# Kernel optimization log

Hardware: AMD Instinct MI355X
Metric: run time of the kernel (lower is better)

Reference implementation:

```python
import jax, jax.numpy as jnp
import numpy as np

H = 8  # num_heads

def setup_inputs() -> dict:
    key = jax.random.key(0)
    k1, k2, k3, k4 = jax.random.split(key, 4)
    B, T, D, K = 16, 8192, 512, 4
    x = jax.random.normal(k1, (B, T, D), dtype=jnp.float32)
    mask = jax.random.randint(k2, (B, T), 0, 2, dtype=jnp.int32)
    queries = jax.random.normal(k3, (1, K, D), dtype=jnp.float32) * 0.02
    # xavier_uniform for (D, D) Linear weight
    limit = np.sqrt(6.0 / (D + D))
    w_out = jax.random.uniform(k4, (D, D), dtype=jnp.float32, minval=-limit, maxval=limit)
    b_out = jnp.zeros((D,), dtype=jnp.float32)
    return {"x": x, "mask": mask, "queries": queries, "w_out": w_out, "b_out": b_out}

def reference(x, mask, queries, w_out, b_out):
    B, T, D = x.shape
    K = queries.shape[1]
    hd = D // H
    scale = jnp.sqrt(jnp.float32(hd))
    q = queries.reshape(K, H, hd)          # shared across batch
    kv = x.reshape(B, T, H, hd)            # keys == values
    scores = jnp.einsum('khd,bthd->bhkt', q, kv) / scale  # (B,H,K,T)
    scores = jnp.where(mask[:, None, None, :] == 0, jnp.float32(-1e9), scores)
    attn = jax.nn.softmax(scores, axis=-1)  # dropout is identity in eval / p=0
    out = jnp.einsum('bhkt,bthd->bkhd', attn, kv).reshape(B, K, D)
    return out @ w_out.T + b_out
```

## Files before the change

### kernel.cpp

```cpp
#include <hip/hip_runtime.h>
#include <math.h>

#define BB 16
#define TT 8192
#define DD 512
#define KK 4
#define HH 8
#define HD 64

__global__ __launch_bounds__(256, 2)
void attn_partial_kernel(const float* __restrict__ x,
                         const int* __restrict__ mask,
                         const float* __restrict__ queries,
                         float* __restrict__ ws,
                         int NC) {
    const int C     = TT / NC;
    const int iters = C >> 3;
    const int b     = blockIdx.x / NC;
    const int c     = blockIdx.x % NC;
    const int t0    = c * C;
    const int tid   = threadIdx.x;
    const int slot  = tid >> 5;
    const int seg   = tid & 31;
    const int h     = seg >> 2;
    const int qd    = seg & 3;

    __shared__ int    smask[512];
    __shared__ float4 smerge[8 * 512];
    __shared__ float  smerge_l[8 * 32];

    for (int i = tid; i < C; i += 256) smask[i] = mask[b * TT + t0 + i];
    __syncthreads();

    const float4* q4 = reinterpret_cast<const float4*>(queries);
    float4 qv[4][4];
    #pragma unroll
    for (int k = 0; k < 4; ++k)
        #pragma unroll
        for (int j = 0; j < 4; ++j) {
            float4 v = q4[k * 128 + seg * 4 + j];
            v.x *= 0.125f; v.y *= 0.125f; v.z *= 0.125f; v.w *= 0.125f;
            qv[k][j] = v;
        }

    float4 av[4][4];
    #pragma unroll
    for (int k = 0; k < 4; ++k)
        #pragma unroll
        for (int j = 0; j < 4; ++j) av[k][j] = make_float4(0.f, 0.f, 0.f, 0.f);
    float l[4] = {0.f, 0.f, 0.f, 0.f};

    const float4* xp = reinterpret_cast<const float4*>(x) +
                       ((size_t)(b * TT + t0 + slot)) * 128 + seg * 4;

    float4 pf[4];
    #pragma unroll
    for (int j = 0; j < 4; ++j) pf[j] = xp[j];
    int mv = smask[slot];

    for (int i = 0; i < iters; ++i) {
        float4 xc[4];
        #pragma unroll
        for (int j = 0; j < 4; ++j) xc[j] = pf[j];
        const int mc = mv;
        if (i + 1 < iters) {
            xp += 1024;
            #pragma unroll
            for (int j = 0; j < 4; ++j) pf[j] = xp[j];
            mv = smask[8 * (i + 1) + slot];
        }

        float s[4];
        #pragma unroll
        for (int k = 0; k < 4; ++k) {
            float a = 0.f;
            #pragma unroll
            for (int j = 0; j < 4; ++j) {
                a = fmaf(qv[k][j].x, xc[j].x, a);
                a = fmaf(qv[k][j].y, xc[j].y, a);
                a = fmaf(qv[k][j].z, xc[j].z, a);
                a = fmaf(qv[k][j].w, xc[j].w, a);
            }
            s[k] = a;
        }
        #pragma unroll
        for (int k = 0; k < 4; ++k) {
            s[k] += __shfl_xor(s[k], 1);
            s[k] += __shfl_xor(s[k], 2);
        }

        float w[4];
        #pragma unroll
        for (int k = 0; k < 4; ++k) w[k] = mc ? __expf(s[k]) : 0.f;
        #pragma unroll
        for (int k = 0; k < 4; ++k) {
            l[k] += w[k];
            #pragma unroll
            for (int j = 0; j < 4; ++j) {
                av[k][j].x = fmaf(w[k], xc[j].x, av[k][j].x);
                av[k][j].y = fmaf(w[k], xc[j].y, av[k][j].y);
                av[k][j].z = fmaf(w[k], xc[j].z, av[k][j].z);
                av[k][j].w = fmaf(w[k], xc[j].w, av[k][j].w);
            }
        }
    }

    #pragma unroll
    for (int k = 0; k < 4; ++k)
        #pragma unroll
        for (int j = 0; j < 4; ++j)
            smerge[slot * 512 + (h * 4 + k) * 16 + qd * 4 + j] = av[k][j];
    if (qd == 0) {
        #pragma unroll
        for (int k = 0; k < 4; ++k) smerge_l[slot * 32 + h * 4 + k] = l[k];
    }
    __syncthreads();

    float4* O4 = reinterpret_cast<float4*>(ws);
    const size_t obase = ((size_t)b * NC + c) * 512;
    for (int f = tid; f < 512; f += 256) {
        float4 sacc = smerge[f];
        #pragma unroll
        for (int s2 = 1; s2 < 8; ++s2) {
            float4 v = smerge[s2 * 512 + f];
            sacc.x += v.x; sacc.y += v.y; sacc.z += v.z; sacc.w += v.w;
        }
        O4[obase + f] = sacc;
    }
    if (tid < 32) {
        float sacc = 0.f;
        #pragma unroll
        for (int s2 = 0; s2 < 8; ++s2) sacc += smerge_l[s2 * 32 + tid];
        float* lp = ws + (size_t)BB * NC * HH * KK * 64;
        lp[(((size_t)b * NC + c) * HH + (tid >> 2)) * KK + (tid & 3)] = sacc;
    }
}

__global__ __launch_bounds__(256, 4)
void merge_gemm_kernel(const float* __restrict__ ws,
                       const float* __restrict__ w_out,
                       const float* __restrict__ b_out,
                       float* __restrict__ out,
                       int NC) {
    const int bk  = blockIdx.x;
    const int b   = bk >> 2;
    const int k   = bk & 3;
    const int tid = threadIdx.x;

    __shared__ __align__(16) float row[512];
    __shared__ float linv[8];

    if (tid < 8) {
        const float* lp = ws + (size_t)BB * NC * HH * KK * 64;
        float s = 0.f;
        for (int c = 0; c < NC; ++c)
            s += lp[(((size_t)b * NC + c) * HH + tid) * KK + k];
        linv[tid] = 1.0f / s;
    }
    __syncthreads();

    for (int item = tid; item < 512; item += 256) {
        const int h = item >> 6, d = item & 63;
        float s = 0.f;
        for (int c = 0; c < NC; ++c)
            s += ws[((((size_t)b * NC + c) * HH + h) * KK + k) * 64 + d];
        row[item] = s * linv[h];
    }
    __syncthreads();

    const float4* W4 = reinterpret_cast<const float4*>(w_out);
    const float4* R4 = reinterpret_cast<const float4*>(row);
    float a0 = b_out[tid];
    float a1 = b_out[tid + 256];
    for (int d4 = 0; d4 < 128; ++d4) {
        const float4 r  = R4[d4];
        const float4 wa = W4[(size_t)tid * 128 + d4];
        const float4 wb = W4[((size_t)tid + 256) * 128 + d4];
        a0 = fmaf(r.x, wa.x, fmaf(r.y, wa.y, fmaf(r.z, wa.z, fmaf(r.w, wa.w, a0))));
        a1 = fmaf(r.x, wb.x, fmaf(r.y, wb.y, fmaf(r.z, wb.z, fmaf(r.w, wb.w, a1))));
    }
    out[(size_t)bk * 512 + tid]       = a0;
    out[(size_t)bk * 512 + tid + 256] = a1;
}

extern "C" void kernel_launch(void* const* d_in, const int* in_sizes, int n_in,
                              void* d_out, int out_size, void* d_ws, size_t ws_size,
                              hipStream_t stream) {
    const float* x       = (const float*)d_in[0];
    const int*   mask    = (const int*)d_in[1];
    const float* queries = (const float*)d_in[2];
    const float* w_out   = (const float*)d_in[3];
    const float* b_out   = (const float*)d_in[4];
    float*       out     = (float*)d_out;
    float*       ws      = (float*)d_ws;

    int NC = 32;
    while (NC > 16 && (size_t)BB * NC * HH * KK * 65 * 4 > ws_size) NC >>= 1;

    attn_partial_kernel<<<BB * NC, 256, 0, stream>>>(x, mask, queries, ws, NC);
    merge_gemm_kernel<<<BB * KK, 256, 0, stream>>>(ws, w_out, b_out, out, NC);
}
```

Baseline: 418.2 us.

## Remap attention threads to one float4 per thread and drop smem merge

Each thread now owns a single float4 of the head dimension and processes two timesteps per block iteration across two halves, instead of four float4s for one timestep, which cuts per-thread query and accumulator registers. That allows launch bounds of 4 blocks per CU. The shared-memory cross-slot merge is removed: each half writes its partials straight to the workspace, and the merge kernel sums over twice as many chunks. The chunk count is also raised to 64 when the workspace allows. The trade-off is more shuffle reductions (16 lanes instead of 4) and more workspace traffic in the merge kernel.

```diff
diff --git a/kernel.cpp b/kernel.cpp
--- a/kernel.cpp
+++ b/kernel.cpp
@@ -8,7 +8,7 @@
 #define HH 8
 #define HD 64
 
-__global__ __launch_bounds__(256, 2)
+__global__ __launch_bounds__(256, 4)
 void attn_partial_kernel(const float* __restrict__ x,
                          const int* __restrict__ mask,
                          const float* __restrict__ queries,
@@ -20,119 +20,88 @@
     const int c     = blockIdx.x % NC;
     const int t0    = c * C;
     const int tid   = threadIdx.x;
-    const int slot  = tid >> 5;
-    const int seg   = tid & 31;
-    const int h     = seg >> 2;
-    const int qd    = seg & 3;
+    const int half  = tid >> 7;
+    const int f     = tid & 127;
+    const int h     = f >> 4;
 
-    __shared__ int    smask[512];
-    __shared__ float4 smerge[8 * 512];
-    __shared__ float  smerge_l[8 * 32];
-
+    __shared__ int smask[512];
     for (int i = tid; i < C; i += 256) smask[i] = mask[b * TT + t0 + i];
     __syncthreads();
 
     const float4* q4 = reinterpret_cast<const float4*>(queries);
-    float4 qv[4][4];
+    float4 qv[4];
     #pragma unroll
-    for (int k = 0; k < 4; ++k)
-        #pragma unroll
-        for (int j = 0; j < 4; ++j) {
-            float4 v = q4[k * 128 + seg * 4 + j];
-            v.x *= 0.125f; v.y *= 0.125f; v.z *= 0.125f; v.w *= 0.125f;
-            qv[k][j] = v;
-        }
+    for (int k = 0; k < 4; ++k) {
+        float4 v = q4[k * 128 + f];
+        v.x *= 0.125f; v.y *= 0.125f; v.z *= 0.125f; v.w *= 0.125f;
+        qv[k] = v;
+    }
 
-    float4 av[4][4];
+    float4 av[4];
     #pragma unroll
-    for (int k = 0; k < 4; ++k)
-        #pragma unroll
-        for (int j = 0; j < 4; ++j) av[k][j] = make_float4(0.f, 0.f, 0.f, 0.f);
+    for (int k = 0; k < 4; ++k) av[k] = make_float4(0.f, 0.f, 0.f, 0.f);
     float l[4] = {0.f, 0.f, 0.f, 0.f};
 
     const float4* xp = reinterpret_cast<const float4*>(x) +
-                       ((size_t)(b * TT + t0 + slot)) * 128 + seg * 4;
+                       ((size_t)(b * TT + t0 + half)) * 128 + f;
 
     float4 pf[4];
+    int    pm[4];
     #pragma unroll
-    for (int j = 0; j < 4; ++j) pf[j] = xp[j];
-    int mv = smask[slot];
+    for (int u = 0; u < 4; ++u) {
+        pf[u] = xp[u * 256];
+        pm[u] = smask[2 * u + half];
+    }
 
     for (int i = 0; i < iters; ++i) {
         float4 xc[4];
+        int    mc[4];
         #pragma unroll
-        for (int j = 0; j < 4; ++j) xc[j] = pf[j];
-        const int mc = mv;
+        for (int u = 0; u < 4; ++u) { xc[u] = pf[u]; mc[u] = pm[u]; }
         if (i + 1 < iters) {
             xp += 1024;
+            const int mbase = 8 * (i + 1) + half;
             #pragma unroll
-            for (int j = 0; j < 4; ++j) pf[j] = xp[j];
-            mv = smask[8 * (i + 1) + slot];
+            for (int u = 0; u < 4; ++u) {
+                pf[u] = xp[u * 256];
+                pm[u] = smask[mbase + 2 * u];
+            }
         }
 
-        float s[4];
         #pragma unroll
-        for (int k = 0; k < 4; ++k) {
-            float a = 0.f;
+        for (int u = 0; u < 4; ++u) {
+            float s[4];
             #pragma unroll
-            for (int j = 0; j < 4; ++j) {
-                a = fmaf(qv[k][j].x, xc[j].x, a);
-                a = fmaf(qv[k][j].y, xc[j].y, a);
-                a = fmaf(qv[k][j].z, xc[j].z, a);
-                a = fmaf(qv[k][j].w, xc[j].w, a);
+            for (int k = 0; k < 4; ++k) {
+                s[k] = fmaf(qv[k].x, xc[u].x,
+                       fmaf(qv[k].y, xc[u].y,
+                       fmaf(qv[k].z, xc[u].z, qv[k].w * xc[u].w)));
             }
-            s[k] = a;
-        }
-        #pragma unroll
-        for (int k = 0; k < 4; ++k) {
-            s[k] += __shfl_xor(s[k], 1);
-            s[k] += __shfl_xor(s[k], 2);
-        }
-
-        float w[4];
-        #pragma unroll
-        for (int k = 0; k < 4; ++k) w[k] = mc ? __expf(s[k]) : 0.f;
-        #pragma unroll
-        for (int k = 0; k < 4; ++k) {
-            l[k] += w[k];
             #pragma unroll
-            for (int j = 0; j < 4; ++j) {
-                av[k][j].x = fmaf(w[k], xc[j].x, av[k][j].x);
-                av[k][j].y = fmaf(w[k], xc[j].y, av[k][j].y);
-                av[k][j].z = fmaf(w[k], xc[j].z, av[k][j].z);
-                av[k][j].w = fmaf(w[k], xc[j].w, av[k][j].w);
+            for (int off = 1; off <= 8; off <<= 1) {
+                #pragma unroll
+                for (int k = 0; k < 4; ++k) s[k] += __shfl_xor(s[k], off);
+            }
+            #pragma unroll
+            for (int k = 0; k < 4; ++k) {
+                const float w = mc[u] ? __expf(s[k]) : 0.f;
+                l[k] += w;
+                av[k].x = fmaf(w, xc[u].x, av[k].x);
+                av[k].y = fmaf(w, xc[u].y, av[k].y);
+                av[k].z = fmaf(w, xc[u].z, av[k].z);
+                av[k].w = fmaf(w, xc[u].w, av[k].w);
             }
         }
     }
 
+    const size_t cid = ((size_t)b * NC + c) * 2 + half;
+    float4* O4 = reinterpret_cast<float4*>(ws);
     #pragma unroll
     for (int k = 0; k < 4; ++k)
-        #pragma unroll
-        for (int j = 0; j < 4; ++j)
-            smerge[slot * 512 + (h * 4 + k) * 16 + qd * 4 + j] = av[k][j];
-    if (qd == 0) {
-        #pragma unroll
-        for (int k = 0; k < 4; ++k) smerge_l[slot * 32 + h * 4 + k] = l[k];
-    }
-    __syncthreads();
-
-    float4* O4 = reinterpret_cast<float4*>(ws);
-    const size_t obase = ((size_t)b * NC + c) * 512;
-    for (int f = tid; f < 512; f += 256) {
-        float4 sacc = smerge[f];
-        #pragma unroll
-        for (int s2 = 1; s2 < 8; ++s2) {
-            float4 v = smerge[s2 * 512 + f];
-            sacc.x += v.x; sacc.y += v.y; sacc.z += v.z; sacc.w += v.w;
-        }
-        O4[obase + f] = sacc;
-    }
-    if (tid < 32) {
-        float sacc = 0.f;
-        #pragma unroll
-        for (int s2 = 0; s2 < 8; ++s2) sacc += smerge_l[s2 * 32 + tid];
-        float* lp = ws + (size_t)BB * NC * HH * KK * 64;
-        lp[(((size_t)b * NC + c) * HH + (tid >> 2)) * KK + (tid & 3)] = sacc;
+        O4[cid * 512 + (h * 4 + k) * 16 + (f & 15)] = av[k];
+    if ((f & 15) == 0) {
+        float4* lp4 = reinterpret_cast<float4*>(ws + (size_t)BB * NC * 2 * 2048);
+        lp4[cid * 8 + h] = make_float4(l[0], l[1], l[2], l[3]);
     }
 }
 
@@ -142,6 +111,7 @@
                        const float* __restrict__ b_out,
                        float* __restrict__ out,
                        int NC) {
+    const int NCC = 2 * NC;
     const int bk  = blockIdx.x;
     const int b   = bk >> 2;
     const int k   = bk & 3;
@@ -151,10 +121,10 @@
     __shared__ float linv[8];
 
     if (tid < 8) {
-        const float* lp = ws + (size_t)BB * NC * HH * KK * 64;
+        const float* lp = ws + (size_t)BB * NCC * 2048;
         float s = 0.f;
-        for (int c = 0; c < NC; ++c)
-            s += lp[(((size_t)b * NC + c) * HH + tid) * KK + k];
+        for (int c2 = 0; c2 < NCC; ++c2)
+            s += lp[((size_t)b * NCC + c2) * 32 + tid * 4 + k];
         linv[tid] = 1.0f / s;
     }
     __syncthreads();
@@ -162,8 +132,8 @@
     for (int item = tid; item < 512; item += 256) {
         const int h = item >> 6, d = item & 63;
         float s = 0.f;
-        for (int c = 0; c < NC; ++c)
-            s += ws[((((size_t)b * NC + c) * HH + h) * KK + k) * 64 + d];
+        for (int c2 = 0; c2 < NCC; ++c2)
+            s += ws[((size_t)b * NCC + c2) * 2048 + (h * 4 + k) * 64 + d];
         row[item] = s * linv[h];
     }
     __syncthreads();
@@ -194,8 +164,8 @@
     float*       out     = (float*)d_out;
     float*       ws      = (float*)d_ws;
 
-    int NC = 32;
-    while (NC > 16 && (size_t)BB * NC * HH * KK * 65 * 4 > ws_size) NC >>= 1;
+    int NC = 64;
+    while (NC > 16 && (size_t)BB * NC * 2 * (2048 + 32) * 4 > ws_size) NC >>= 1;
 
     attn_partial_kernel<<<BB * NC, 256, 0, stream>>>(x, mask, queries, ws, NC);
     merge_gemm_kernel<<<BB * KK, 256, 0, stream>>>(ws, w_out, b_out, out, NC);
```

Result: slower. 488.3 us (+16.7%).
